# Kernel optimization log

Hardware: AMD Instinct MI355X
Metric: run time of the kernel (lower is better)

Reference implementation:

```python
import jax, jax.numpy as jnp
import numpy as np
from jax import lax

BETA = 1e-07
LAMBDA_TV = 1e-08


def _resize_bilinear_ac(x, out_h, out_w):
    """Bilinear resize with align_corners=True, NCHW layout (matches F.interpolate)."""
    B, C, H, W = x.shape
    ys = jnp.arange(out_h, dtype=jnp.float32) * ((H - 1) / max(out_h - 1, 1))
    xs = jnp.arange(out_w, dtype=jnp.float32) * ((W - 1) / max(out_w - 1, 1))
    y0 = jnp.floor(ys).astype(jnp.int32); y1 = jnp.minimum(y0 + 1, H - 1)
    x0 = jnp.floor(xs).astype(jnp.int32); x1 = jnp.minimum(x0 + 1, W - 1)
    wy = (ys - y0.astype(jnp.float32))[:, None]   # [out_h,1]
    wx = (xs - x0.astype(jnp.float32))[None, :]   # [1,out_w]
    r0 = x[:, :, y0, :]; r1 = x[:, :, y1, :]      # [B,C,out_h,W]
    top = r0[:, :, :, x0] * (1.0 - wx) + r0[:, :, :, x1] * wx
    bot = r1[:, :, :, x0] * (1.0 - wx) + r1[:, :, :, x1] * wx
    return top * (1.0 - wy) + bot * wy


def _levelset_loss(output, target):
    B = output.shape[0]
    # pcentroid computed under no_grad in torch -> stop_gradient here
    num = jnp.einsum('bthw,bchw->btc', target, output)
    den = jnp.sum(output, axis=(2, 3))                       # [B,C]
    pcent = lax.stop_gradient(num / den[:, None, :])          # [B,T,C]
    plevel = target[:, :, None, :, :] - pcent[:, :, :, None, None]  # [B,T,C,H,W]
    return jnp.sum(plevel * plevel * output[:, None]) / B


def _gradient_loss2d(output):
    B = output.shape[0]
    dH = jnp.abs(output[:, :, 1:, :] - output[:, :, :-1, :])
    dW = jnp.abs(output[:, :, :, 1:] - output[:, :, :, :-1])
    return (jnp.sum(dH) + jnp.sum(dW)) / B


def _nonlocal_tv_loss(f_output, f_sem):
    B, Cs, H, W = f_sem.shape
    N = H * W
    fo = _resize_bilinear_ac(f_output, H, W)                  # [B,C,H,W]
    C = fo.shape[1]
    # F.normalize(f_sem, dim=1) (eps=1e-12)
    norm = jnp.sqrt(jnp.sum(f_sem * f_sem, axis=1, keepdims=True))
    sem = f_sem / jnp.maximum(norm, 1e-12)
    sem_f = sem.reshape(B, Cs, N)
    # tau[b,r,p] = relu(<sem_r, sem_p>); normalized by global spatial max per (b,r)
    tau = jax.nn.relu(jnp.einsum('bcr,bcp->brp', sem_f, sem_f))  # [B,N,N]
    tau_max = jnp.max(tau, axis=2, keepdims=True)
    tau_n = tau / (tau_max + 1e-05)
    # torch.matmul(dL[B,C,H,W], tau[B,1,H,W]) summed over everything reduces to
    # sum_{i,k,j} dL[b,c,i,k] * tau[b,k,j] = sum_k (sum_i dL[b,c,i,k]) * (sum_j tau[b,k,j])
    t = tau_n.reshape(B, N, H, W).sum(axis=3)                 # [B,N,H] row-sums of tau
    of = fo.reshape(B, C, N)
    # dL[b,c,r,h,w] = |out_r - out_{(h,w)}| (penalty='l1')
    dL = jnp.abs(of[:, :, :, None, None] - fo[:, :, None, :, :])  # [B,C,N,H,W]
    A = dL.sum(axis=3)                                         # [B,C,N,W] sum over rows i
    return jnp.einsum('bcrk,brk->', A, t) / B


def setup_inputs() -> dict:
    key = jax.random.key(0)
    k1, k2, k3, k4 = jax.random.split(key, 4)
    return {
        'output': jax.random.uniform(k1, (4, 21, 512, 512), dtype=jnp.float32),
        'target': jax.random.uniform(k2, (4, 3, 512, 512), dtype=jnp.float32),
        'f_sem': jax.random.normal(k3, (4, 256, 32, 32), dtype=jnp.float32),
        'f_output': jax.random.uniform(k4, (4, 21, 64, 64), dtype=jnp.float32),
        'use_NonLocal_TV': 1,
    }


def reference(output, target, f_sem, f_output, use_NonLocal_TV):
    loss_LS = _levelset_loss(output, target)
    if use_NonLocal_TV:
        loss_TV = _nonlocal_tv_loss(f_output, f_sem) * LAMBDA_TV
    else:
        loss_TV = _gradient_loss2d(output) * LAMBDA_TV
    loss_MS = (loss_LS + loss_TV) * BETA
    return (loss_LS * BETA, loss_TV * BETA, loss_MS)
```

## Files before the change

kernel.cpp:

```cpp
#include <hip/hip_runtime.h>

#define BETA_F   1e-7f
#define LAMBDA_F 1e-8f

#define HWSZ 262144
#define NBC  84
#define NPIX 1024

#define OFF_FO    0
#define OFF_GSUM  86016
#define OFF_INVN  (86016 + 131072)
#define OFF_RMAX  (217088 + 4096)
#define OFF_LS    (221184 + 4096)
#define OFF_ACC   (225280 + 588)
#define ZERO_START OFF_RMAX
#define ZERO_COUNT (4096 + 588 + 4)

#define N_GRAM_BLK 144

__device__ const unsigned char RT_[36] =
    {0,0,0,0,0,0,0,0, 1,1,1,1,1,1,1, 2,2,2,2,2,2, 3,3,3,3,3, 4,4,4,4, 5,5,5, 6,6, 7};
__device__ const unsigned char CT_[36] =
    {0,1,2,3,4,5,6,7, 1,2,3,4,5,6,7, 2,3,4,5,6,7, 3,4,5,6,7, 4,5,6,7, 5,6,7, 6,7, 7};

__global__ __launch_bounds__(256) void k_prep(const float* __restrict__ fo_in,
                                              const float* __restrict__ fsem,
                                              float* __restrict__ ws) {
    const int bid = blockIdx.x, tid = threadIdx.x;
    if (bid < 19) {
        int i = bid * 256 + tid;
        if (i < ZERO_COUNT) ws[ZERO_START + i] = 0.f;
    } else if (bid < 103) {
        const int bc = bid - 19;
        const float* im = fo_in + bc * 4096;
        for (int p = tid; p < 1024; p += 256) {
            const int oy = p >> 5, ox = p & 31;
            const float R = 63.0f / 31.0f;
            float sy = oy * R, sx = ox * R;
            int y0 = (int)sy, x0 = (int)sx;
            int y1 = min(y0 + 1, 63), x1 = min(x0 + 1, 63);
            float wy = sy - (float)y0, wx = sx - (float)x0;
            float v00 = im[y0 * 64 + x0], v01 = im[y0 * 64 + x1];
            float v10 = im[y1 * 64 + x0], v11 = im[y1 * 64 + x1];
            float top = v00 * (1.f - wx) + v01 * wx;
            float bot = v10 * (1.f - wx) + v11 * wx;
            ws[OFF_FO + bc * NPIX + p] = top * (1.f - wy) + bot * wy;
        }
    } else {
        const int blk = bid - 103;
        const int b = blk >> 4, pg = blk & 15;
        const int p0 = pg * 64;
        const int pi = tid & 63, cg = tid >> 6;
        float s = 0.f;
        for (int c = cg; c < 256; c += 4) {
            float v = fsem[(b * 256 + c) * 1024 + p0 + pi];
            s += v * v;
        }
        __shared__ float red[4][64];
        red[cg][pi] = s;
        __syncthreads();
        if (tid < 64) {
            float t = red[0][tid] + red[1][tid] + red[2][tid] + red[3][tid];
            ws[OFF_INVN + b * 1024 + p0 + tid] = 1.f / fmaxf(sqrtf(t), 1e-12f);
        }
    }
}

__device__ __forceinline__ int swz(int p4, int k) {
    int s = (p4 >> 1) | ((p4 & 1) << 4);
    return s ^ (k & 7);
}

__device__ __forceinline__ void acc_px(float4 o, float4 ta, float4 tb, float4 tc,
                                       float& dn, float& n0, float& n1, float& n2,
                                       float& q0, float& q1, float& q2) {
    dn += o.x + o.y + o.z + o.w;
    n0 += ta.x*o.x + ta.y*o.y + ta.z*o.z + ta.w*o.w;
    q0 += ta.x*ta.x*o.x + ta.y*ta.y*o.y + ta.z*ta.z*o.z + ta.w*ta.w*o.w;
    n1 += tb.x*o.x + tb.y*o.y + tb.z*o.z + tb.w*o.w;
    q1 += tb.x*tb.x*o.x + tb.y*tb.y*o.y + tb.z*tb.z*o.z + tb.w*tb.w*o.w;
    n2 += tc.x*o.x + tc.y*o.y + tc.z*o.z + tc.w*o.w;
    q2 += tc.x*tc.x*o.x + tc.y*tc.y*o.y + tc.z*tc.z*o.z + tc.w*tc.w*o.w;
}

__global__ __launch_bounds__(256) void k_main(const float* __restrict__ outp,
                                              const float* __restrict__ tgt,
                                              const float* __restrict__ fsem,
                                              float* __restrict__ ws) {
    __shared__ __align__(16) char smem[21504];
    const int tid = threadIdx.x;

    if (blockIdx.x < N_GRAM_BLK) {
        float4* As4    = (float4*)smem;
        float4* Bs4    = (float4*)(smem + 8192);
        float*  gs_row = (float*)(smem + 16384);
        float*  gs_col = (float*)(smem + 18432);
        int*    rm_row = (int*)(smem + 20480);
        int*    rm_col = (int*)(smem + 20992);
        const int bid = blockIdx.x;
        const int b = bid / 36, t = bid % 36;
        const int rt = RT_[t], ct = CT_[t];
        const bool diag = (rt == ct);
        const int r0 = rt * 128, c0 = ct * 128;
        for (int i = tid; i < 512; i += 256) { gs_row[i] = 0.f; gs_col[i] = 0.f; }
        if (tid < 128) { rm_row[tid] = 0; rm_col[tid] = 0; }

        const int tr = tid >> 4, tc = tid & 15;
        float acc[8][8];
        #pragma unroll
        for (int i = 0; i < 8; ++i)
            #pragma unroll
            for (int j = 0; j < 8; ++j) acc[i][j] = 0.f;

        const int kl = tid >> 5, p4s = tid & 31;
        for (int kk = 0; kk < 16; ++kk) {
            __syncthreads();
            #pragma unroll
            for (int q = 0; q < 2; ++q) {
                int k = kl + q * 8;
                const float* srcA = &fsem[(b * 256 + kk * 16 + k) * 1024 + r0 + p4s * 4];
                const float* srcB = &fsem[(b * 256 + kk * 16 + k) * 1024 + c0 + p4s * 4];
                float4 va = *(const float4*)srcA;
                float4 vb = *(const float4*)srcB;
                int sl = swz(p4s, k);
                As4[k * 32 + sl] = va;
                Bs4[k * 32 + sl] = vb;
            }
            __syncthreads();
            #pragma unroll 4
            for (int k = 0; k < 16; ++k) {
                int k7 = k & 7;
                float4 a0 = As4[k * 32 + (tr ^ k7)];
                float4 a1 = As4[k * 32 + ((tr ^ k7) | 16)];
                float4 b0 = Bs4[k * 32 + (tc ^ k7)];
                float4 b1 = Bs4[k * 32 + ((tc ^ k7) | 16)];
                float a[8]  = {a0.x, a0.y, a0.z, a0.w, a1.x, a1.y, a1.z, a1.w};
                float bb[8] = {b0.x, b0.y, b0.z, b0.w, b1.x, b1.y, b1.z, b1.w};
                #pragma unroll
                for (int i = 0; i < 8; ++i)
                    #pragma unroll
                    for (int j = 0; j < 8; ++j)
                        acc[i][j] += a[i] * bb[j];
            }
        }

        float ir[8], ic[8];
        #pragma unroll
        for (int i = 0; i < 8; ++i) {
            ir[i] = ws[OFF_INVN + b * 1024 + r0 + tr * 8 + i];
            ic[i] = ws[OFF_INVN + b * 1024 + c0 + tc * 8 + i];
        }
        const int gr = tc >> 2;
        #pragma unroll
        for (int i = 0; i < 8; ++i) {
            float s = 0.f, m = 0.f;
            #pragma unroll
            for (int j = 0; j < 8; ++j) {
                float v = fmaxf(acc[i][j], 0.f) * ir[i] * ic[j];
                s += v;
                m = fmaxf(m, v);
            }
            int row = tr * 8 + i;
            atomicAdd(&gs_row[row * 4 + gr], s);
            atomicMax(&rm_row[row], __float_as_int(m));
        }
        if (!diag) {
            const int gc = tr >> 2;
            #pragma unroll
            for (int j = 0; j < 8; ++j) {
                float s = 0.f, m = 0.f;
                #pragma unroll
                for (int i = 0; i < 8; ++i) {
                    float v = fmaxf(acc[i][j], 0.f) * ir[i] * ic[j];
                    s += v;
                    m = fmaxf(m, v);
                }
                int col = tc * 8 + j;
                atomicAdd(&gs_col[col * 4 + gc], s);
                atomicMax(&rm_col[col], __float_as_int(m));
            }
        }
        __syncthreads();
        for (int i = tid; i < 512; i += 256) {
            int row = i >> 2, gg = i & 3;
            ws[OFF_GSUM + (b * 1024 + r0 + row) * 32 + ct * 4 + gg] = gs_row[i];
            if (!diag)
                ws[OFF_GSUM + (b * 1024 + c0 + row) * 32 + rt * 4 + gg] = gs_col[i];
        }
        if (tid < 128) {
            atomicMax((int*)&ws[OFF_RMAX + b * 1024 + r0 + tid], rm_row[tid]);
            if (!diag)
                atomicMax((int*)&ws[OFF_RMAX + b * 1024 + c0 + tid], rm_col[tid]);
        }
    } else {
        float (*red)[7] = (float (*)[7])smem;
        const int blk = blockIdx.x - N_GRAM_BLK;
        const int slice = blk & 31, bc = blk >> 5;
        const int b = bc / 21;
        const float4* o4 = (const float4*)(outp + (size_t)bc * HWSZ + slice * 8192);
        const float4* t4 = (const float4*)(tgt + (size_t)b * (3 * HWSZ) + slice * 8192);
        float dn = 0, n0 = 0, n1 = 0, n2 = 0, q0 = 0, q1 = 0, q2 = 0;
        #pragma unroll
        for (int half = 0; half < 2; ++half) {
            float4 o[4], ta[4], tb[4], tc[4];
            #pragma unroll
            for (int j = 0; j < 4; ++j) {
                const int i = tid + (half * 4 + j) * 256;
                o[j]  = o4[i];
                ta[j] = t4[i];
                tb[j] = t4[i + 65536];
                tc[j] = t4[i + 131072];
            }
            #pragma unroll
            for (int j = 0; j < 4; ++j)
                acc_px(o[j], ta[j], tb[j], tc[j], dn, n0, n1, n2, q0, q1, q2);
        }
        float vals[7] = {n0, n1, n2, q0, q1, q2, dn};
        #pragma unroll
        for (int j = 0; j < 7; ++j) {
            float v = vals[j];
            #pragma unroll
            for (int off = 32; off; off >>= 1) v += __shfl_xor(v, off);
            if ((tid & 63) == 0) red[tid >> 6][j] = v;
        }
        __syncthreads();
        if (tid < 7) {
            float s = red[0][tid] + red[1][tid] + red[2][tid] + red[3][tid];
            atomicAdd(&ws[OFF_LS + bc * 7 + tid], s);
        }
    }
}

__global__ __launch_bounds__(256) void k_tv(const float* __restrict__ ws,
                                            float* __restrict__ acc_out) {
    const int bc = blockIdx.y;
    const int b = bc / 21;
    const int tid = threadIdx.x;
    __shared__ float4 fo4[256];
    const float4* src = (const float4*)(ws + OFF_FO + bc * NPIX);
    fo4[tid] = src[tid];
    __syncthreads();
    const int r = blockIdx.x * 256 + tid;
    const float v = ((const float*)fo4)[r];
    float ak[32];
    #pragma unroll
    for (int k = 0; k < 32; ++k) ak[k] = 0.f;
    #pragma unroll 4
    for (int h = 0; h < 32; ++h) {
        #pragma unroll
        for (int k4 = 0; k4 < 8; ++k4) {
            float4 f = fo4[h * 8 + k4];
            ak[k4 * 4 + 0] += fabsf(v - f.x);
            ak[k4 * 4 + 1] += fabsf(v - f.y);
            ak[k4 * 4 + 2] += fabsf(v - f.z);
            ak[k4 * 4 + 3] += fabsf(v - f.w);
        }
    }
    const float rm = ws[OFF_RMAX + b * 1024 + r];
    const float inv = 1.f / (rm + 1e-5f);
    const float* t = ws + OFF_GSUM + (b * 1024 + r) * 32;
    float dot = 0.f;
    #pragma unroll
    for (int k = 0; k < 32; ++k) dot += ak[k] * t[k];
    float part = dot * inv;
    #pragma unroll
    for (int off = 32; off; off >>= 1) part += __shfl_xor(part, off);
    __shared__ float red[4];
    if ((tid & 63) == 0) red[tid >> 6] = part;
    __syncthreads();
    if (tid == 0) atomicAdd(acc_out, red[0] + red[1] + red[2] + red[3]);
}

__global__ void k_combine(const float* __restrict__ ws, float* __restrict__ out) {
    const int tid = threadIdx.x;
    float v = 0.f;
    if (tid < NBC) {
        const float* p = ws + OFF_LS + tid * 7;
        float den = p[6];
        v = (p[3] + p[4] + p[5]) - (p[0]*p[0] + p[1]*p[1] + p[2]*p[2]) / den;
    }
    #pragma unroll
    for (int off = 32; off; off >>= 1) v += __shfl_xor(v, off);
    __shared__ float red[2];
    if ((tid & 63) == 0) red[tid >> 6] = v;
    __syncthreads();
    if (tid == 0) {
        float lsv = (red[0] + red[1]) * 0.25f;
        float tvv = ws[OFF_ACC] * 0.25f;
        out[0] = lsv * BETA_F;
        out[1] = tvv * LAMBDA_F * BETA_F;
        out[2] = (lsv + tvv * LAMBDA_F) * BETA_F;
    }
}

extern "C" void kernel_launch(void* const* d_in, const int* in_sizes, int n_in,
                              void* d_out, int out_size, void* d_ws, size_t ws_size,
                              hipStream_t stream) {
    const float* output   = (const float*)d_in[0];
    const float* target   = (const float*)d_in[1];
    const float* f_sem    = (const float*)d_in[2];
    const float* f_output = (const float*)d_in[3];
    float* ws  = (float*)d_ws;
    float* out = (float*)d_out;

    hipLaunchKernelGGL(k_prep,    dim3(167),             dim3(256), 0, stream, f_output, f_sem, ws);
    hipLaunchKernelGGL(k_main,    dim3(N_GRAM_BLK+2688), dim3(256), 0, stream, output, target, f_sem, ws);
    hipLaunchKernelGGL(k_tv,      dim3(4, 84),           dim3(256), 0, stream, ws, ws + OFF_ACC);
    hipLaunchKernelGGL(k_combine, dim3(1),               dim3(128), 0, stream, ws, out);
}
```

Measured before the change: 217.3 us.

## Stage target tile in LDS and reuse across all 21 channels per block

Restructures the level-set reduction so each block loads a 1024-pixel slice of the three target channels into shared memory once, then loops warps over the 21 output channels reusing it. Before, every (batch, channel) block re-read the target from global memory, so target traffic was multiplied 21 times. Partial sums are now spread over 8 slots per statistic to reduce atomic contention, with the combine kernel summing the slots. The workspace offsets and zeroing range grow to match. Block count drops from 2688 to 1024, and each block does less memory-level parallelism per channel.

Measured after the change: 221.6 us. Within noise of the previous version (+2.0%).

```diff
diff --git a/kernel.cpp b/kernel.cpp
--- a/kernel.cpp
+++ b/kernel.cpp
@@ -12,11 +12,12 @@
 #define OFF_INVN  (86016 + 131072)
 #define OFF_RMAX  (217088 + 4096)
 #define OFF_LS    (221184 + 4096)
-#define OFF_ACC   (225280 + 588)
+#define OFF_ACC   (225280 + 4704)
 #define ZERO_START OFF_RMAX
-#define ZERO_COUNT (4096 + 588 + 4)
+#define ZERO_COUNT (4096 + 4704 + 4)
 
 #define N_GRAM_BLK 144
+#define N_LS_BLK   1024
 
 __device__ const unsigned char RT_[36] =
     {0,0,0,0,0,0,0,0, 1,1,1,1,1,1,1, 2,2,2,2,2,2, 3,3,3,3,3, 4,4,4,4, 5,5,5, 6,6, 7};
@@ -27,11 +28,11 @@
                                               const float* __restrict__ fsem,
                                               float* __restrict__ ws) {
     const int bid = blockIdx.x, tid = threadIdx.x;
-    if (bid < 19) {
+    if (bid < 35) {
         int i = bid * 256 + tid;
         if (i < ZERO_COUNT) ws[ZERO_START + i] = 0.f;
-    } else if (bid < 103) {
-        const int bc = bid - 19;
+    } else if (bid < 119) {
+        const int bc = bid - 35;
         const float* im = fo_in + bc * 4096;
         for (int p = tid; p < 1024; p += 256) {
             const int oy = p >> 5, ox = p & 31;
@@ -47,7 +48,7 @@
             ws[OFF_FO + bc * NPIX + p] = top * (1.f - wy) + bot * wy;
         }
     } else {
-        const int blk = bid - 103;
+        const int blk = bid - 119;
         const int b = blk >> 4, pg = blk & 15;
         const int p0 = pg * 64;
         const int pi = tid & 63, cg = tid >> 6;
@@ -193,40 +194,45 @@
                 atomicMax((int*)&ws[OFF_RMAX + b * 1024 + c0 + tid], rm_col[tid]);
         }
     } else {
-        float (*red)[7] = (float (*)[7])smem;
+        float* tls = (float*)smem;
         const int blk = blockIdx.x - N_GRAM_BLK;
-        const int slice = blk & 31, bc = blk >> 5;
-        const int b = bc / 21;
-        const float4* o4 = (const float4*)(outp + (size_t)bc * HWSZ + slice * 8192);
-        const float4* t4 = (const float4*)(tgt + (size_t)b * (3 * HWSZ) + slice * 8192);
-        float dn = 0, n0 = 0, n1 = 0, n2 = 0, q0 = 0, q1 = 0, q2 = 0;
-        #pragma unroll
-        for (int half = 0; half < 2; ++half) {
-            float4 o[4], ta[4], tb[4], tc[4];
-            #pragma unroll
-            for (int j = 0; j < 4; ++j) {
-                const int i = tid + (half * 4 + j) * 256;
-                o[j]  = o4[i];
-                ta[j] = t4[i];
-                tb[j] = t4[i + 65536];
-                tc[j] = t4[i + 131072];
-            }
-            #pragma unroll
-            for (int j = 0; j < 4; ++j)
-                acc_px(o[j], ta[j], tb[j], tc[j], dn, n0, n1, n2, q0, q1, q2);
-        }
-        float vals[7] = {n0, n1, n2, q0, q1, q2, dn};
-        #pragma unroll
-        for (int j = 0; j < 7; ++j) {
-            float v = vals[j];
-            #pragma unroll
-            for (int off = 32; off; off >>= 1) v += __shfl_xor(v, off);
-            if ((tid & 63) == 0) red[tid >> 6][j] = v;
+        const int b = blk >> 8, s = blk & 255;
+        const size_t tbase = (size_t)b * (3 * HWSZ) + s * 1024 + tid * 4;
+        #pragma unroll
+        for (int ch = 0; ch < 3; ++ch) {
+            float4 tv = *(const float4*)(tgt + tbase + (size_t)ch * HWSZ);
+            *(float4*)(tls + ch * 1024 + tid * 4) = tv;
         }
         __syncthreads();
-        if (tid < 7) {
-            float s = red[0][tid] + red[1][tid] + red[2][tid] + red[3][tid];
-            atomicAdd(&ws[OFF_LS + bc * 7 + tid], s);
+        const int w = tid >> 6, lane = tid & 63;
+        for (int c = w; c < 21; c += 4) {
+            const float* obase = outp + (size_t)(b * 21 + c) * HWSZ + s * 1024;
+            float4 o[4], t0[4], t1[4], t2[4];
+            #pragma unroll
+            for (int i = 0; i < 4; ++i)
+                o[i] = *(const float4*)(obase + i * 256 + lane * 4);
+            #pragma unroll
+            for (int i = 0; i < 4; ++i) {
+                const int p = i * 256 + lane * 4;
+                t0[i] = *(const float4*)(tls + p);
+                t1[i] = *(const float4*)(tls + 1024 + p);
+                t2[i] = *(const float4*)(tls + 2048 + p);
+            }
+            float dn = 0, n0 = 0, n1 = 0, n2 = 0, q0 = 0, q1 = 0, q2 = 0;
+            #pragma unroll
+            for (int i = 0; i < 4; ++i)
+                acc_px(o[i], t0[i], t1[i], t2[i], dn, n0, n1, n2, q0, q1, q2);
+            float vals[7] = {n0, n1, n2, q0, q1, q2, dn};
+            float myv = 0.f;
+            #pragma unroll
+            for (int q = 0; q < 7; ++q) {
+                float v = vals[q];
+                #pragma unroll
+                for (int off = 32; off; off >>= 1) v += __shfl_xor(v, off);
+                if (lane == q) myv = v;
+            }
+            if (lane < 7)
+                atomicAdd(&ws[OFF_LS + (b * 21 + c) * 56 + lane * 8 + (s & 7)], myv);
         }
     }
 }
@@ -275,9 +281,17 @@
     const int tid = threadIdx.x;
     float v = 0.f;
     if (tid < NBC) {
-        const float* p = ws + OFF_LS + tid * 7;
-        float den = p[6];
-        v = (p[3] + p[4] + p[5]) - (p[0]*p[0] + p[1]*p[1] + p[2]*p[2]) / den;
+        const float* p = ws + OFF_LS + tid * 56;
+        float vv[7];
+        #pragma unroll
+        for (int q = 0; q < 7; ++q) {
+            float s = 0.f;
+            #pragma unroll
+            for (int k = 0; k < 8; ++k) s += p[q * 8 + k];
+            vv[q] = s;
+        }
+        float den = vv[6];
+        v = (vv[3] + vv[4] + vv[5]) - (vv[0]*vv[0] + vv[1]*vv[1] + vv[2]*vv[2]) / den;
     }
     #pragma unroll
     for (int off = 32; off; off >>= 1) v += __shfl_xor(v, off);
@@ -303,8 +317,8 @@
     float* ws  = (float*)d_ws;
     float* out = (float*)d_out;
 
-    hipLaunchKernelGGL(k_prep,    dim3(167),             dim3(256), 0, stream, f_output, f_sem, ws);
-    hipLaunchKernelGGL(k_main,    dim3(N_GRAM_BLK+2688), dim3(256), 0, stream, output, target, f_sem, ws);
-    hipLaunchKernelGGL(k_tv,      dim3(4, 84),           dim3(256), 0, stream, ws, ws + OFF_ACC);
-    hipLaunchKernelGGL(k_combine, dim3(1),               dim3(128), 0, stream, ws, out);
-}
+    hipLaunchKernelGGL(k_prep,    dim3(183),               dim3(256), 0, stream, f_output, f_sem, ws);
+    hipLaunchKernelGGL(k_main,    dim3(N_GRAM_BLK+N_LS_BLK), dim3(256), 0, stream, output, target, f_sem, ws);
+    hipLaunchKernelGGL(k_tv,      dim3(4, 84),             dim3(256), 0, stream, ws, ws + OFF_ACC);
+    hipLaunchKernelGGL(k_combine, dim3(1),                 dim3(128), 0, stream, ws, out);
+}
```

## Compute semantic Gram tiles with bf16 MFMA instead of scalar FP32 FMA

Applied to the files above, without the earlier changes.

Replaces the FP32 register-tiled outer-product Gram matrix in the gram blocks with bf16 MFMA 16x16x32 instructions. Inputs are converted to bf16 while being staged into padded, transposed LDS tiles. Row and column sum/max reductions now use wave shuffles and write straight to global, replacing the shared-memory atomics. This targets the compute-bound scalar FMA loop, at the cost of bf16 precision in the similarity values and more scattered global atomicMax traffic.

New measurement: 198.9 us. 1.09x faster.

```diff
diff --git a/kernel.cpp b/kernel.cpp
--- a/kernel.cpp
+++ b/kernel.cpp
@@ -18,10 +18,19 @@
 
 #define N_GRAM_BLK 144
 
+typedef __attribute__((ext_vector_type(8))) short short8;
+typedef __attribute__((ext_vector_type(4))) float f32x4;
+
 __device__ const unsigned char RT_[36] =
     {0,0,0,0,0,0,0,0, 1,1,1,1,1,1,1, 2,2,2,2,2,2, 3,3,3,3,3, 4,4,4,4, 5,5,5, 6,6, 7};
 __device__ const unsigned char CT_[36] =
     {0,1,2,3,4,5,6,7, 1,2,3,4,5,6,7, 2,3,4,5,6,7, 3,4,5,6,7, 4,5,6,7, 5,6,7, 6,7, 7};
+
+__device__ __forceinline__ unsigned short bf16r(float f) {
+    unsigned int u = __float_as_uint(f);
+    u += 0x7fffu + ((u >> 16) & 1u);
+    return (unsigned short)(u >> 16);
+}
 
 __global__ __launch_bounds__(256) void k_prep(const float* __restrict__ fo_in,
                                               const float* __restrict__ fsem,
@@ -66,11 +75,6 @@
     }
 }
 
-__device__ __forceinline__ int swz(int p4, int k) {
-    int s = (p4 >> 1) | ((p4 & 1) << 4);
-    return s ^ (k & 7);
-}
-
 __device__ __forceinline__ void acc_px(float4 o, float4 ta, float4 tb, float4 tc,
                                        float& dn, float& n0, float& n1, float& n2,
                                        float& q0, float& q1, float& q2) {
@@ -83,114 +87,132 @@
     q2 += tc.x*tc.x*o.x + tc.y*tc.y*o.y + tc.z*tc.z*o.z + tc.w*tc.w*o.w;
 }
 
+#define LSTR 40
+
 __global__ __launch_bounds__(256) void k_main(const float* __restrict__ outp,
                                               const float* __restrict__ tgt,
                                               const float* __restrict__ fsem,
                                               float* __restrict__ ws) {
-    __shared__ __align__(16) char smem[21504];
+    __shared__ __align__(16) char smem[20480];
     const int tid = threadIdx.x;
 
     if (blockIdx.x < N_GRAM_BLK) {
-        float4* As4    = (float4*)smem;
-        float4* Bs4    = (float4*)(smem + 8192);
-        float*  gs_row = (float*)(smem + 16384);
-        float*  gs_col = (float*)(smem + 18432);
-        int*    rm_row = (int*)(smem + 20480);
-        int*    rm_col = (int*)(smem + 20992);
+        unsigned short* Asub = (unsigned short*)smem;
+        unsigned short* Bsub = (unsigned short*)(smem + 10240);
         const int bid = blockIdx.x;
         const int b = bid / 36, t = bid % 36;
         const int rt = RT_[t], ct = CT_[t];
         const bool diag = (rt == ct);
         const int r0 = rt * 128, c0 = ct * 128;
-        for (int i = tid; i < 512; i += 256) { gs_row[i] = 0.f; gs_col[i] = 0.f; }
-        if (tid < 128) { rm_row[tid] = 0; rm_col[tid] = 0; }
-
-        const int tr = tid >> 4, tc = tid & 15;
-        float acc[8][8];
-        #pragma unroll
-        for (int i = 0; i < 8; ++i)
-            #pragma unroll
-            for (int j = 0; j < 8; ++j) acc[i][j] = 0.f;
-
-        const int kl = tid >> 5, p4s = tid & 31;
-        for (int kk = 0; kk < 16; ++kk) {
+
+        const int ch_l = tid & 31, pxg = tid >> 5;
+        const int w = tid >> 6, l = tid & 63;
+        const int wr = (w >> 1) * 64, wc = (w & 1) * 64;
+        const int lr = l & 15, lg = l >> 4;
+
+        f32x4 acc[4][4];
+        #pragma unroll
+        for (int i = 0; i < 4; ++i)
+            #pragma unroll
+            for (int j = 0; j < 4; ++j) acc[i][j] = (f32x4){0.f, 0.f, 0.f, 0.f};
+
+        for (int kk = 0; kk < 8; ++kk) {
             __syncthreads();
-            #pragma unroll
-            for (int q = 0; q < 2; ++q) {
-                int k = kl + q * 8;
-                const float* srcA = &fsem[(b * 256 + kk * 16 + k) * 1024 + r0 + p4s * 4];
-                const float* srcB = &fsem[(b * 256 + kk * 16 + k) * 1024 + c0 + p4s * 4];
-                float4 va = *(const float4*)srcA;
-                float4 vb = *(const float4*)srcB;
-                int sl = swz(p4s, k);
-                As4[k * 32 + sl] = va;
-                Bs4[k * 32 + sl] = vb;
+            const float* fb = fsem + (size_t)(b * 256 + kk * 32 + ch_l) * 1024;
+            #pragma unroll
+            for (int q = 0; q < 4; ++q) {
+                float4 va = *(const float4*)(fb + r0 + pxg * 16 + q * 4);
+                float4 vb = *(const float4*)(fb + c0 + pxg * 16 + q * 4);
+                const int px = pxg * 16 + q * 4;
+                Asub[(px + 0) * LSTR + ch_l] = bf16r(va.x);
+                Asub[(px + 1) * LSTR + ch_l] = bf16r(va.y);
+                Asub[(px + 2) * LSTR + ch_l] = bf16r(va.z);
+                Asub[(px + 3) * LSTR + ch_l] = bf16r(va.w);
+                Bsub[(px + 0) * LSTR + ch_l] = bf16r(vb.x);
+                Bsub[(px + 1) * LSTR + ch_l] = bf16r(vb.y);
+                Bsub[(px + 2) * LSTR + ch_l] = bf16r(vb.z);
+                Bsub[(px + 3) * LSTR + ch_l] = bf16r(vb.w);
             }
             __syncthreads();
-            #pragma unroll 4
-            for (int k = 0; k < 16; ++k) {
-                int k7 = k & 7;
-                float4 a0 = As4[k * 32 + (tr ^ k7)];
-                float4 a1 = As4[k * 32 + ((tr ^ k7) | 16)];
-                float4 b0 = Bs4[k * 32 + (tc ^ k7)];
-                float4 b1 = Bs4[k * 32 + ((tc ^ k7) | 16)];
-                float a[8]  = {a0.x, a0.y, a0.z, a0.w, a1.x, a1.y, a1.z, a1.w};
-                float bb[8] = {b0.x, b0.y, b0.z, b0.w, b1.x, b1.y, b1.z, b1.w};
-                #pragma unroll
-                for (int i = 0; i < 8; ++i)
-                    #pragma unroll
-                    for (int j = 0; j < 8; ++j)
-                        acc[i][j] += a[i] * bb[j];
+            short8 a8[4], b8[4];
+            #pragma unroll
+            for (int fr = 0; fr < 4; ++fr)
+                a8[fr] = *(const short8*)(Asub + (wr + fr * 16 + lr) * LSTR + lg * 8);
+            #pragma unroll
+            for (int fc = 0; fc < 4; ++fc)
+                b8[fc] = *(const short8*)(Bsub + (wc + fc * 16 + lr) * LSTR + lg * 8);
+            #pragma unroll
+            for (int fr = 0; fr < 4; ++fr)
+                #pragma unroll
+                for (int fc = 0; fc < 4; ++fc)
+                    acc[fr][fc] = __builtin_amdgcn_mfma_f32_16x16x32_bf16(
+                        a8[fr], b8[fc], acc[fr][fc], 0, 0, 0);
+        }
+
+        float ir[4][4], ic[4];
+        #pragma unroll
+        for (int fr = 0; fr < 4; ++fr)
+            #pragma unroll
+            for (int rg = 0; rg < 4; ++rg)
+                ir[fr][rg] = ws[OFF_INVN + b * 1024 + r0 + wr + fr * 16 + lg * 4 + rg];
+        #pragma unroll
+        for (int fc = 0; fc < 4; ++fc)
+            ic[fc] = ws[OFF_INVN + b * 1024 + c0 + wc + fc * 16 + lr];
+        #pragma unroll
+        for (int fr = 0; fr < 4; ++fr)
+            #pragma unroll
+            for (int fc = 0; fc < 4; ++fc)
+                #pragma unroll
+                for (int rg = 0; rg < 4; ++rg)
+                    acc[fr][fc][rg] = fmaxf(acc[fr][fc][rg], 0.f) * ir[fr][rg] * ic[fc];
+
+        #pragma unroll
+        for (int fr = 0; fr < 4; ++fr)
+            #pragma unroll
+            for (int rg = 0; rg < 4; ++rg) {
+                float v0 = acc[fr][0][rg] + acc[fr][1][rg];
+                float v1 = acc[fr][2][rg] + acc[fr][3][rg];
+                float m  = fmaxf(fmaxf(acc[fr][0][rg], acc[fr][1][rg]),
+                                 fmaxf(acc[fr][2][rg], acc[fr][3][rg]));
+                #pragma unroll
+                for (int msk = 1; msk < 16; msk <<= 1) {
+                    v0 += __shfl_xor(v0, msk);
+                    v1 += __shfl_xor(v1, msk);
+                    m = fmaxf(m, __shfl_xor(m, msk));
+                }
+                if (lr == 0) {
+                    const int row = r0 + wr + fr * 16 + lg * 4 + rg;
+                    float* g = ws + OFF_GSUM + (size_t)(b * 1024 + row) * 32
+                             + ct * 4 + (w & 1) * 2;
+                    g[0] = v0; g[1] = v1;
+                    atomicMax((int*)&ws[OFF_RMAX + b * 1024 + row], __float_as_int(m));
+                }
             }
-        }
-
-        float ir[8], ic[8];
-        #pragma unroll
-        for (int i = 0; i < 8; ++i) {
-            ir[i] = ws[OFF_INVN + b * 1024 + r0 + tr * 8 + i];
-            ic[i] = ws[OFF_INVN + b * 1024 + c0 + tc * 8 + i];
-        }
-        const int gr = tc >> 2;
-        #pragma unroll
-        for (int i = 0; i < 8; ++i) {
-            float s = 0.f, m = 0.f;
-            #pragma unroll
-            for (int j = 0; j < 8; ++j) {
-                float v = fmaxf(acc[i][j], 0.f) * ir[i] * ic[j];
-                s += v;
-                m = fmaxf(m, v);
+        if (!diag) {
+            #pragma unroll
+            for (int fc = 0; fc < 4; ++fc) {
+                float c0s = 0.f, c1s = 0.f, cm = 0.f;
+                #pragma unroll
+                for (int rg = 0; rg < 4; ++rg) {
+                    c0s += acc[0][fc][rg] + acc[1][fc][rg];
+                    c1s += acc[2][fc][rg] + acc[3][fc][rg];
+                    cm = fmaxf(cm, fmaxf(fmaxf(acc[0][fc][rg], acc[1][fc][rg]),
+                                         fmaxf(acc[2][fc][rg], acc[3][fc][rg])));
+                }
+                #pragma unroll
+                for (int msk = 16; msk < 64; msk <<= 1) {
+                    c0s += __shfl_xor(c0s, msk);
+                    c1s += __shfl_xor(c1s, msk);
+                    cm = fmaxf(cm, __shfl_xor(cm, msk));
+                }
+                if (lg == 0) {
+                    const int col = c0 + wc + fc * 16 + lr;
+                    float* g = ws + OFF_GSUM + (size_t)(b * 1024 + col) * 32
+                             + rt * 4 + (w >> 1) * 2;
+                    g[0] = c0s; g[1] = c1s;
+                    atomicMax((int*)&ws[OFF_RMAX + b * 1024 + col], __float_as_int(cm));
+                }
             }
-            int row = tr * 8 + i;
-            atomicAdd(&gs_row[row * 4 + gr], s);
-            atomicMax(&rm_row[row], __float_as_int(m));
-        }
-        if (!diag) {
-            const int gc = tr >> 2;
-            #pragma unroll
-            for (int j = 0; j < 8; ++j) {
-                float s = 0.f, m = 0.f;
-                #pragma unroll
-                for (int i = 0; i < 8; ++i) {
-                    float v = fmaxf(acc[i][j], 0.f) * ir[i] * ic[j];
-                    s += v;
-                    m = fmaxf(m, v);
-                }
-                int col = tc * 8 + j;
-                atomicAdd(&gs_col[col * 4 + gc], s);
-                atomicMax(&rm_col[col], __float_as_int(m));
-            }
-        }
-        __syncthreads();
-        for (int i = tid; i < 512; i += 256) {
-            int row = i >> 2, gg = i & 3;
-            ws[OFF_GSUM + (b * 1024 + r0 + row) * 32 + ct * 4 + gg] = gs_row[i];
-            if (!diag)
-                ws[OFF_GSUM + (b * 1024 + c0 + row) * 32 + rt * 4 + gg] = gs_col[i];
-        }
-        if (tid < 128) {
-            atomicMax((int*)&ws[OFF_RMAX + b * 1024 + r0 + tid], rm_row[tid]);
-            if (!diag)
-                atomicMax((int*)&ws[OFF_RMAX + b * 1024 + c0 + tid], rm_col[tid]);
         }
     } else {
         float (*red)[7] = (float (*)[7])smem;
```
